# Kernel optimization log

Hardware: AMD Instinct MI355X
Metric: run time of the kernel (lower is better)

## Reference

```python
import jax, jax.numpy as jnp
import numpy as np

B, T, C = 4, 2048, 768
NH, NKV, HD = 12, 12, 64
RMS_EPS = 1e-6


def rms_norm(x):
    return x * jax.lax.rsqrt(jnp.mean(x * x, axis=-1, keepdims=True) + RMS_EPS)


def apply_rotary_emb(x, cos, sin):
    # x: [B,T,H,D], cos/sin: [T,D/2]
    d2 = x.shape[-1] // 2
    x1, x2 = x[..., :d2], x[..., d2:]
    c = cos[None, :, None, :]
    s = sin[None, :, None, :]
    return jnp.concatenate([x1 * c - x2 * s, x1 * s + x2 * c], axis=-1)


def setup_inputs() -> dict:
    key = jax.random.key(0)
    ks = jax.random.split(key, 10)
    inv_freq = 1.0 / (100000.0 ** (np.arange(0, HD, 2, dtype=np.float32) / HD))  # [HD/2]
    t = np.arange(T, dtype=np.float32)
    freqs = np.outer(t, inv_freq)  # [T, HD/2]
    return {
        "x": jax.random.normal(ks[0], (B, T, C), jnp.float32),
        "ve": jax.random.normal(ks[1], (B, T, C), jnp.float32),
        "cos": jnp.asarray(np.cos(freqs)),
        "sin": jnp.asarray(np.sin(freqs)),
        "Wq": jax.random.normal(ks[2], (C, C), jnp.float32) * (1.0 / np.sqrt(C)),
        "Wk": jax.random.normal(ks[3], (C, C), jnp.float32) * (1.0 / np.sqrt(C)),
        "Wv": jax.random.normal(ks[4], (C, C), jnp.float32) * (1.0 / np.sqrt(C)),
        "Wproj": jax.random.normal(ks[5], (C, C), jnp.float32) * (1.0 / np.sqrt(C)),
        "Wgate": jax.random.normal(ks[6], (NKV, 12), jnp.float32) * 0.1,
        "window_left": 1024,
    }


def reference(x, ve, cos, sin, Wq, Wk, Wv, Wproj, Wgate, window_left):
    q = (x @ Wq.T).reshape(B, T, NH, HD)
    k = (x @ Wk.T).reshape(B, T, NKV, HD)
    v = (x @ Wv.T).reshape(B, T, NKV, HD)

    # value-embedding gating (has_ve path): gate = 3*sigmoid(Linear(x[...,:12]))
    ve_h = ve.reshape(B, T, NKV, HD)
    gate = 3.0 * jax.nn.sigmoid(x[..., :12] @ Wgate.T)  # [B,T,NKV]
    v = v + gate[..., None] * ve_h

    q = apply_rotary_emb(q, cos, sin)
    k = apply_rotary_emb(k, cos, sin)
    q = rms_norm(q) * 1.2
    k = rms_norm(k) * 1.2

    # sliding-window causal bias
    row = jnp.arange(T)[:, None]
    col = jnp.arange(T)[None, :]
    mask = (row >= col) & ((row - col) <= window_left)
    bias = jnp.where(mask, 0.0, -1e9).astype(x.dtype)  # [T,T]

    scale = 1.0 / np.sqrt(HD)
    att = jnp.einsum("bqhd,bkhd->bhqk", q, k) * scale + bias[None, None]
    att = jax.nn.softmax(att, axis=-1)
    y = jnp.einsum("bhqk,bkhd->bqhd", att, v).reshape(B, T, C)
    return y @ Wproj.T
```

## Files before the change

kernel.cpp:

```cpp
#include <hip/hip_runtime.h>
#include <hip/hip_bf16.h>
#include <cstdint>
#include <cstddef>

#define B_  4
#define T_  2048
#define C_  768
#define NH_ 12
#define HD_ 64

typedef __bf16 bf16_t;
typedef __attribute__((ext_vector_type(8))) __bf16 bf16x8;
typedef __attribute__((ext_vector_type(4))) __bf16 bf16x4;
typedef __attribute__((ext_vector_type(4))) float floatx4;
typedef __attribute__((ext_vector_type(8))) unsigned short ushort8;
typedef __attribute__((ext_vector_type(4))) unsigned int uint4v;

#define MFMA16(a, b, c) __builtin_amdgcn_mfma_f32_16x16x32_bf16((a), (b), (c), 0, 0, 0)

#define SM_C1 0.18033688f
#define SM_C2 -17.3123405f

typedef const __attribute__((address_space(1))) uint8_t* gptr_t;
typedef __attribute__((address_space(3))) uint8_t* lptr_t;

static __device__ __forceinline__ void gld16(const void* g, void* l) {
    __builtin_amdgcn_global_load_lds((gptr_t)g, (lptr_t)l, 16, 0, 0);
}

__global__ __launch_bounds__(256) void cvt_all_kernel(
    const void* s0, const void* s1, const void* s2, const void* s3,
    const void* s4, const void* s5, const void* s6, const void* s7, const void* s8,
    bf16_t* d0, bf16_t* d1, bf16_t* d2, bf16_t* d3,
    bf16_t* d4, bf16_t* d5, bf16_t* d6, bf16_t* d7, bf16_t* d8)
{
    const void* srcs[9] = {s0, s1, s2, s3, s4, s5, s6, s7, s8};
    bf16_t*     dsts[9] = {d0, d1, d2, d3, d4, d5, d6, d7, d8};
    const int   ns[9]   = {B_*T_*C_, B_*T_*C_, T_*32, T_*32,
                           C_*C_, C_*C_, C_*C_, C_*C_, 144};
    const int t = blockIdx.y;
    const void* src = srcs[t];
    bf16_t*     dst = dsts[t];
    const int   nc  = ns[t] >> 3;
    const bool isf32 = (((const unsigned short*)s2)[0] == 0);
    const int stride = gridDim.x * 256;
    if (isf32) {
        const float* sf = (const float*)src;
        for (int i = blockIdx.x * 256 + threadIdx.x; i < nc; i += stride) {
            ushort8 o;
#pragma unroll
            for (int j = 0; j < 8; j++)
                o[j] = (unsigned short)__builtin_bit_cast(unsigned short,
                         (bf16_t)sf[i * 8 + j]);
            *(ushort8*)&dst[i * 8] = o;
        }
    } else {
        const uint4v* sb = (const uint4v*)src;
        uint4v* db = (uint4v*)dst;
        for (int i = blockIdx.x * 256 + threadIdx.x; i < nc; i += stride)
            db[i] = sb[i];
    }
}

template <bool OUT_BF16>
__device__ __forceinline__ void gemm_bt_tile(
    const bf16_t* __restrict__ A, const bf16_t* __restrict__ Bm,
    void* __restrict__ Cout, int m0, int n0, int K, int ldc)
{
    __shared__ bf16_t As[2][128 * 32];
    __shared__ bf16_t Bs[2][128 * 32];
    const int tid  = threadIdx.x;
    const int lane = tid & 63;
    const int wid  = tid >> 6;
    const int m16  = lane & 15;
    const int quad = lane >> 4;
    const int wm   = (wid >> 1) * 64;
    const int wn   = (wid & 1) * 64;
    const int srow = lane >> 2;
    const int soct = (lane & 3) * 8;

    floatx4 acc[4][4];
#pragma unroll
    for (int i = 0; i < 4; i++)
#pragma unroll
        for (int j = 0; j < 4; j++) acc[i][j] = (floatx4){0.f, 0.f, 0.f, 0.f};

    for (int k0 = 0; k0 < K; k0 += 64) {
        const bf16_t* ga0 = &A[(size_t)(m0 + 16 * wid + srow) * K + k0 + soct];
        const bf16_t* gb0 = &Bm[(size_t)(n0 + 16 * wid + srow) * K + k0 + soct];
        gld16(ga0,                       (bf16_t*)As[0] + wid * 512);
        gld16(ga0 + (size_t)64 * K,      (bf16_t*)As[0] + wid * 512 + 2048);
        gld16(gb0,                       (bf16_t*)Bs[0] + wid * 512);
        gld16(gb0 + (size_t)64 * K,      (bf16_t*)Bs[0] + wid * 512 + 2048);
        gld16(ga0 + 32,                  (bf16_t*)As[1] + wid * 512);
        gld16(ga0 + (size_t)64 * K + 32, (bf16_t*)As[1] + wid * 512 + 2048);
        gld16(gb0 + 32,                  (bf16_t*)Bs[1] + wid * 512);
        gld16(gb0 + (size_t)64 * K + 32, (bf16_t*)Bs[1] + wid * 512 + 2048);
        __syncthreads();
#pragma unroll
        for (int half = 0; half < 2; half++) {
            bf16x8 af[4], bfr[4];
#pragma unroll
            for (int i = 0; i < 4; i++)
                af[i] = *(const bf16x8*)&As[half][(wm + i * 16 + m16) * 32 + quad * 8];
#pragma unroll
            for (int j = 0; j < 4; j++)
                bfr[j] = *(const bf16x8*)&Bs[half][(wn + j * 16 + m16) * 32 + quad * 8];
#pragma unroll
            for (int i = 0; i < 4; i++)
#pragma unroll
                for (int j = 0; j < 4; j++)
                    acc[i][j] = MFMA16(af[i], bfr[j], acc[i][j]);
        }
        __syncthreads();
    }

#pragma unroll
    for (int i = 0; i < 4; i++) {
#pragma unroll
        for (int j = 0; j < 4; j++) {
            const int colg = n0 + wn + j * 16 + m16;
#pragma unroll
            for (int r = 0; r < 4; r++) {
                const int rowg = m0 + wm + i * 16 + quad * 4 + r;
                if (OUT_BF16)
                    ((bf16_t*)Cout)[(size_t)rowg * ldc + colg] = (bf16_t)acc[i][j][r];
                else
                    ((float*)Cout)[(size_t)rowg * ldc + colg] = acc[i][j][r];
            }
        }
    }
}

__global__ __launch_bounds__(256) void gemm_qkv_kernel(
    const bf16_t* __restrict__ xb,
    const bf16_t* __restrict__ wq, const bf16_t* __restrict__ wk,
    const bf16_t* __restrict__ wv,
    bf16_t* __restrict__ ql, bf16_t* __restrict__ kl, bf16_t* __restrict__ vl)
{
    const int sel = blockIdx.y / 6;
    const int nt  = blockIdx.y % 6;
    const bf16_t* Bm = (sel == 0) ? wq : (sel == 1) ? wk : wv;
    bf16_t* Cout     = (sel == 0) ? ql : (sel == 1) ? kl : vl;
    gemm_bt_tile<true>(xb, Bm, Cout, blockIdx.x * 128, nt * 128, C_, C_);
}

__global__ __launch_bounds__(256) void gemm_proj_kernel(
    const bf16_t* __restrict__ yb, const bf16_t* __restrict__ wp,
    void* __restrict__ out, const void* cos_raw)
{
    const bool isf32 = (((const unsigned short*)cos_raw)[0] == 0);
    if (isf32)
        gemm_bt_tile<false>(yb, wp, out, blockIdx.x * 128, blockIdx.y * 128, C_, C_);
    else
        gemm_bt_tile<true>(yb, wp, out, blockIdx.x * 128, blockIdx.y * 128, C_, C_);
}

__global__ __launch_bounds__(256) void qkv_post_kernel(
    const bf16_t* __restrict__ x, const bf16_t* __restrict__ ve,
    const bf16_t* __restrict__ cosp, const bf16_t* __restrict__ sinp,
    const bf16_t* __restrict__ wg,
    const bf16_t* __restrict__ ql, const bf16_t* __restrict__ kl,
    const bf16_t* __restrict__ vl,
    bf16_t* __restrict__ qb, bf16_t* __restrict__ kb, bf16_t* __restrict__ vt)
{
    const int t0 = blockIdx.x * 32;
    const int b  = blockIdx.y;
    const int w  = threadIdx.x >> 6;
    const int h  = blockIdx.z * 4 + w;
    const int d  = threadIdx.x & 63;
    __shared__ float vtile[4][32 * 65];
    float* vt_l = vtile[w];
    const float wgd = (d < 12) ? (float)wg[h * 12 + d] : 0.f;

    for (int c = 0; c < 32; c++) {
        const int t  = t0 + c;
        const int bt = b * T_ + t;
        const size_t lin = (size_t)bt * C_ + h * HD_ + d;
        float gx = (d < 12) ? (float)x[(size_t)bt * C_ + d] * wgd : 0.f;
        gx += __shfl_xor(gx, 1, 64); gx += __shfl_xor(gx, 2, 64);
        gx += __shfl_xor(gx, 4, 64); gx += __shfl_xor(gx, 8, 64);
        gx = __shfl(gx, 0, 64);
        const float gate = 3.f / (1.f + __expf(-gx));
        vt_l[c * 65 + d] = (float)vl[lin] + gate * (float)ve[lin];

        const float co = (float)cosp[t * 32 + (d & 31)];
        const float si = (float)sinp[t * 32 + (d & 31)];
        const size_t oidx = ((size_t)(b * NH_ + h) * T_ + t) * HD_ + d;
        {
            const float own = (float)ql[lin];
            const float oth = __shfl_xor(own, 32, 64);
            const float qr  = (d < 32) ? (own * co - oth * si) : (oth * si + own * co);
            float ss = qr * qr;
#pragma unroll
            for (int off = 1; off < 64; off <<= 1) ss += __shfl_xor(ss, off, 64);
            qb[oidx] = (bf16_t)(qr * rsqrtf(ss * (1.f / 64.f) + 1e-6f) * 1.2f);
        }
        {
            const float own = (float)kl[lin];
            const float oth = __shfl_xor(own, 32, 64);
            const float kr  = (d < 32) ? (own * co - oth * si) : (oth * si + own * co);
            float ss = kr * kr;
#pragma unroll
            for (int off = 1; off < 64; off <<= 1) ss += __shfl_xor(ss, off, 64);
            kb[oidx] = (bf16_t)(kr * rsqrtf(ss * (1.f / 64.f) + 1e-6f) * 1.2f);
        }
    }

    const int cc = threadIdx.x & 31;
    const int dh = (threadIdx.x >> 5) & 1;
    const int tp = t0 + ((((cc >> 2) & 3) << 3) | ((cc >> 4) << 2) | (cc & 3));
#pragma unroll 4
    for (int it = 0; it < 32; it++) {
        const int dd = it * 2 + dh;
        vt[((size_t)(b * NH_ + h) * HD_ + dd) * T_ + tp] =
            (bf16_t)vt_l[cc * 65 + dd];
    }
}

__global__ __launch_bounds__(256, 3) void attn_kernel(
    const bf16_t* __restrict__ Q, const bf16_t* __restrict__ Km,
    const bf16_t* __restrict__ Vtg, bf16_t* __restrict__ Y,
    const int* __restrict__ wl)
{
    const int bx   = blockIdx.x;
    const int bh   = blockIdx.y;
    const int gsel = bh >> 4;
    int qblk;
    if (gsel == 0)      qblk = bx;
    else if (gsel == 1) qblk = 15 - bx;
    else                qblk = (int)((0xECA8642013579BDFull >> (bx * 4)) & 0xF);
    const int q0 = qblk * 128;
    const int b  = bh / NH_;
    const int h  = bh % NH_;
    const int window = wl[0];
    const int tid  = threadIdx.x;
    const int wid  = tid >> 6;
    const int lane = tid & 63;
    const int m16  = lane & 15;
    const int quad = lane >> 4;
    const int qw   = q0 + wid * 32;

    const size_t base = (size_t)bh * T_ * HD_;
    const bf16_t* Qb  = Q + base;
    const bf16_t* Kb  = Km + base;
    const bf16_t* Vb  = Vtg + base;

    __shared__ bf16_t Ks[2][64 * 64];
    __shared__ bf16_t Vs[2][64 * 64];

    bf16x8 qf[2][2];
#pragma unroll
    for (int mt = 0; mt < 2; mt++)
#pragma unroll
        for (int ks = 0; ks < 2; ks++)
            qf[mt][ks] = *(const bf16x8*)
                &Qb[(size_t)(qw + mt * 16 + m16) * HD_ + ks * 32 + quad * 8];

    const int srow = tid >> 2;
    const int soct = tid & 3;
    const int g0   = 2 * soct, g1 = 2 * soct + 1;
    const int kd0  = srow * 64 + ((g0 ^ (srow & 7)) << 3);
    const int kd1  = srow * 64 + ((g1 ^ (srow & 7)) << 3);
    int rsw[2];
#pragma unroll
    for (int ks = 0; ks < 2; ks++)
        rsw[ks] = (((ks * 4 + quad) ^ (m16 & 7)) << 3);

    int lo = q0 - window;
    if (lo < 0) lo = 0;
    lo &= ~63;
    const int nch = (q0 + 128 - lo) >> 6;

    floatx4 accO[2][4];
#pragma unroll
    for (int mt = 0; mt < 2; mt++)
#pragma unroll
        for (int dt = 0; dt < 4; dt++) accO[mt][dt] = (floatx4){0.f, 0.f, 0.f, 0.f};
    float lsum[2] = {0.f, 0.f};
    const bf16x4 zero4 = {(bf16_t)0.f, (bf16_t)0.f, (bf16_t)0.f, (bf16_t)0.f};

    bf16x8 ka0 = *(const bf16x8*)&Kb[(size_t)(lo + srow) * HD_ + g0 * 8];
    bf16x8 ka1 = *(const bf16x8*)&Kb[(size_t)(lo + srow) * HD_ + g1 * 8];
    bf16x8 va0 = *(const bf16x8*)&Vb[(size_t)srow * T_ + lo + g0 * 8];
    bf16x8 va1 = *(const bf16x8*)&Vb[(size_t)srow * T_ + lo + g1 * 8];
    *(bf16x8*)&Ks[0][kd0] = ka0;
    *(bf16x8*)&Ks[0][kd1] = ka1;
    *(bf16x8*)&Vs[0][kd0] = va0;
    *(bf16x8*)&Vs[0][kd1] = va1;

    for (int ic = 0; ic < nch; ic++) {
        const int kc = lo + ic * 64;
        const bool more = (ic + 1 < nch);
        if (more) {
            const int kn = kc + 64;
            ka0 = *(const bf16x8*)&Kb[(size_t)(kn + srow) * HD_ + g0 * 8];
            ka1 = *(const bf16x8*)&Kb[(size_t)(kn + srow) * HD_ + g1 * 8];
            va0 = *(const bf16x8*)&Vb[(size_t)srow * T_ + kn + g0 * 8];
            va1 = *(const bf16x8*)&Vb[(size_t)srow * T_ + kn + g1 * 8];
        }
        __syncthreads();
        const int buf = ic & 1;

        const bool skip = (kc > qw + 31) || (kc + 63 < qw - window);
        if (!skip) {
            bf16x8 kf[4][2];
#pragma unroll
            for (int nt = 0; nt < 4; nt++) {
                const int rb = (nt * 16 + m16) * 64;
                kf[nt][0] = *(const bf16x8*)&Ks[buf][rb + rsw[0]];
                kf[nt][1] = *(const bf16x8*)&Ks[buf][rb + rsw[1]];
            }
            bf16x4 pk[2][4];
            unsigned livemask = 0;
#pragma unroll
            for (int mt = 0; mt < 2; mt++) {
                const int qmin = qw + mt * 16, qmax = qmin + 15;
                float lacc = 0.f;
#pragma unroll
                for (int nt = 0; nt < 4; nt++) {
                    const int kmin = kc + nt * 16, kmax = kmin + 15;
                    if (kmin > qmax || kmax < qmin - window) {
                        pk[mt][nt] = zero4;
                        continue;
                    }
                    livemask |= 1u << (mt * 4 + nt);
                    floatx4 z = (floatx4){0.f, 0.f, 0.f, 0.f};
                    z = MFMA16(kf[nt][0], qf[mt][0], z);
                    z = MFMA16(kf[nt][1], qf[mt][1], z);
                    const bool edge = (kmax > qmin) || (kmin < qmax - window);
                    const int query = qmin + m16;
                    bf16x4 t4;
#pragma unroll
                    for (int r = 0; r < 4; r++) {
                        float p = __builtin_amdgcn_exp2f(
                            fmaf(z[r], SM_C1, SM_C2));
                        if (edge) {
                            const int key = kmin + quad * 4 + r;
                            const bool ok = (key <= query) &&
                                            (query - key <= window);
                            p = ok ? p : 0.f;
                        }
                        t4[r] = (bf16_t)p;
                        lacc += p;
                    }
                    pk[mt][nt] = t4;
                }
                lsum[mt] += lacc;
            }
#pragma unroll
            for (int pr = 0; pr < 2; pr++) {
                const unsigned pm0 = (livemask >> (2 * pr)) & 3u;
                const unsigned pm1 = (livemask >> (4 + 2 * pr)) & 3u;
                if (!(pm0 | pm1)) continue;
                const bf16x8 pa0 = __builtin_shufflevector(
                    pk[0][2 * pr], pk[0][2 * pr + 1], 0, 1, 2, 3, 4, 5, 6, 7);
                const bf16x8 pa1 = __builtin_shufflevector(
                    pk[1][2 * pr], pk[1][2 * pr + 1], 0, 1, 2, 3, 4, 5, 6, 7);
                const int vco = (((pr * 4 + quad) ^ (m16 & 7)) << 3);
#pragma unroll
                for (int dt = 0; dt < 4; dt++) {
                    const bf16x8 vf = *(const bf16x8*)
                        &Vs[buf][(dt * 16 + m16) * 64 + vco];
                    if (pm0) accO[0][dt] = MFMA16(pa0, vf, accO[0][dt]);
                    if (pm1) accO[1][dt] = MFMA16(pa1, vf, accO[1][dt]);
                }
            }
        }

        if (more) {
            const int nb = buf ^ 1;
            *(bf16x8*)&Ks[nb][kd0] = ka0;
            *(bf16x8*)&Ks[nb][kd1] = ka1;
            *(bf16x8*)&Vs[nb][kd0] = va0;
            *(bf16x8*)&Vs[nb][kd1] = va1;
        }
    }

#pragma unroll
    for (int mt = 0; mt < 2; mt++) {
        float red = lsum[mt];
        red += __shfl_xor(red, 16, 64);
        red += __shfl_xor(red, 32, 64);
#pragma unroll
        for (int r = 0; r < 4; r++) {
            const float lq  = __shfl(red, quad * 4 + r, 64);
            const float inv = 1.f / lq;
            const int   tq  = qw + mt * 16 + quad * 4 + r;
#pragma unroll
            for (int dt = 0; dt < 4; dt++)
                Y[((size_t)b * T_ + tq) * C_ + h * HD_ + dt * 16 + m16] =
                    (bf16_t)(accO[mt][dt][r] * inv);
        }
    }
}

extern "C" void kernel_launch(void* const* d_in, const int* in_sizes, int n_in,
                              void* d_out, int out_size, void* d_ws, size_t ws_size,
                              hipStream_t stream)
{
    const void* x_raw   = d_in[0];
    const void* ve_raw  = d_in[1];
    const void* cos_raw = d_in[2];
    const void* sin_raw = d_in[3];
    const void* wq_raw  = d_in[4];
    const void* wk_raw  = d_in[5];
    const void* wv_raw  = d_in[6];
    const void* wp_raw  = d_in[7];
    const void* wg_raw  = d_in[8];
    const int*  wl      = (const int*)d_in[9];

    const size_t NTC = (size_t)B_ * T_ * C_;
    const size_t WSZ = (size_t)C_ * C_;

    bf16_t* ws  = (bf16_t*)d_ws;
    bf16_t* xb  = ws;
    bf16_t* veb = xb + NTC;
    bf16_t* cb  = veb + NTC;
    bf16_t* sb  = cb + T_ * 32;
    bf16_t* wqb = sb + T_ * 32;
    bf16_t* wkb = wqb + WSZ;
    bf16_t* wvb = wkb + WSZ;
    bf16_t* wpb = wvb + WSZ;
    bf16_t* wgb = wpb + WSZ;
    bf16_t* ql  = wgb + 256;
    bf16_t* kl  = ql + NTC;
    bf16_t* vl  = kl + NTC;
    bf16_t* qb  = vl + NTC;
    bf16_t* kb  = qb + NTC;
    bf16_t* vt  = kb + NTC;
    bf16_t* yb  = ql;

    cvt_all_kernel<<<dim3(1024, 9), 256, 0, stream>>>(
        x_raw, ve_raw, cos_raw, sin_raw, wq_raw, wk_raw, wv_raw, wp_raw, wg_raw,
        xb, veb, cb, sb, wqb, wkb, wvb, wpb, wgb);

    gemm_qkv_kernel<<<dim3(64, 18), 256, 0, stream>>>(xb, wqb, wkb, wvb, ql, kl, vl);

    qkv_post_kernel<<<dim3(T_ / 32, B_, 3), 256, 0, stream>>>(
        xb, veb, cb, sb, wgb, ql, kl, vl, qb, kb, vt);

    attn_kernel<<<dim3(16, 48), 256, 0, stream>>>(qb, kb, vt, yb, wl);

    gemm_proj_kernel<<<dim3(64, 6), 256, 0, stream>>>(yb, wpb, d_out, cos_raw);
}
```

Baseline: 257.3 us.

## Fuse RoPE, RMSNorm and value gating into QKV GEMM epilogue

Removes the separate qkv_post kernel. The QKV GEMM epilogue now applies rotary embedding and RMSNorm to Q/K inside registers, using a shuffle reduction across the 64-wide head. For V it adds the sigmoid-gated value embedding and writes the transposed layout. Attention now reads Q/K in the [B,T,C] layout, and the conversion kernel is skipped when inputs are already bf16. This removes a full round trip of the Q, K and V intermediates through global memory, at the cost of a heavier GEMM epilogue and strided attention loads.

```diff
diff --git a/kernel.cpp b/kernel.cpp
--- a/kernel.cpp
+++ b/kernel.cpp
@@ -14,7 +14,6 @@
 typedef __attribute__((ext_vector_type(4))) __bf16 bf16x4;
 typedef __attribute__((ext_vector_type(4))) float floatx4;
 typedef __attribute__((ext_vector_type(8))) unsigned short ushort8;
-typedef __attribute__((ext_vector_type(4))) unsigned int uint4v;
 
 #define MFMA16(a, b, c) __builtin_amdgcn_mfma_f32_16x16x32_bf16((a), (b), (c), 0, 0, 0)
 
@@ -26,6 +25,13 @@
 
 static __device__ __forceinline__ void gld16(const void* g, void* l) {
     __builtin_amdgcn_global_load_lds((gptr_t)g, (lptr_t)l, 16, 0, 0);
+}
+
+static __device__ __forceinline__ float bfl(unsigned p) {
+    return __builtin_bit_cast(float, p << 16);
+}
+static __device__ __forceinline__ float bfh(unsigned p) {
+    return __builtin_bit_cast(float, p & 0xffff0000u);
 }
 
 __global__ __launch_bounds__(256) void cvt_all_kernel(
@@ -34,31 +40,191 @@
     bf16_t* d0, bf16_t* d1, bf16_t* d2, bf16_t* d3,
     bf16_t* d4, bf16_t* d5, bf16_t* d6, bf16_t* d7, bf16_t* d8)
 {
+    const bool isf32 = (((const unsigned short*)s2)[0] == 0);
+    if (!isf32) return;
     const void* srcs[9] = {s0, s1, s2, s3, s4, s5, s6, s7, s8};
     bf16_t*     dsts[9] = {d0, d1, d2, d3, d4, d5, d6, d7, d8};
     const int   ns[9]   = {B_*T_*C_, B_*T_*C_, T_*32, T_*32,
                            C_*C_, C_*C_, C_*C_, C_*C_, 144};
     const int t = blockIdx.y;
-    const void* src = srcs[t];
+    const float* sf = (const float*)srcs[t];
     bf16_t*     dst = dsts[t];
     const int   nc  = ns[t] >> 3;
-    const bool isf32 = (((const unsigned short*)s2)[0] == 0);
     const int stride = gridDim.x * 256;
-    if (isf32) {
-        const float* sf = (const float*)src;
-        for (int i = blockIdx.x * 256 + threadIdx.x; i < nc; i += stride) {
-            ushort8 o;
-#pragma unroll
-            for (int j = 0; j < 8; j++)
-                o[j] = (unsigned short)__builtin_bit_cast(unsigned short,
-                         (bf16_t)sf[i * 8 + j]);
-            *(ushort8*)&dst[i * 8] = o;
+    for (int i = blockIdx.x * 256 + threadIdx.x; i < nc; i += stride) {
+        ushort8 o;
+#pragma unroll
+        for (int j = 0; j < 8; j++)
+            o[j] = (unsigned short)__builtin_bit_cast(unsigned short,
+                     (bf16_t)sf[i * 8 + j]);
+        *(ushort8*)&dst[i * 8] = o;
+    }
+}
+
+__global__ __launch_bounds__(256) void gemm_qkv_fused(
+    const void* xr,  const bf16_t* xc,
+    const void* wqr, const bf16_t* wqc,
+    const void* wkr, const bf16_t* wkc,
+    const void* wvr, const bf16_t* wvc,
+    const void* cr,  const bf16_t* ccv,
+    const void* sr,  const bf16_t* scv,
+    const void* ver, const bf16_t* vec,
+    const void* wgr, const bf16_t* wgc,
+    bf16_t* qn, bf16_t* kn, bf16_t* vt)
+{
+    __shared__ alignas(16) char sm[36864];
+    const bool f32 = (((const unsigned short*)cr)[0] == 0);
+    const bf16_t* X  = f32 ? xc  : (const bf16_t*)xr;
+    const bf16_t* WQ = f32 ? wqc : (const bf16_t*)wqr;
+    const bf16_t* WK = f32 ? wkc : (const bf16_t*)wkr;
+    const bf16_t* WV = f32 ? wvc : (const bf16_t*)wvr;
+    const bf16_t* CC = f32 ? ccv : (const bf16_t*)cr;
+    const bf16_t* SS = f32 ? scv : (const bf16_t*)sr;
+    const bf16_t* VE = f32 ? vec : (const bf16_t*)ver;
+    const bf16_t* WG = f32 ? wgc : (const bf16_t*)wgr;
+
+    const int sel = blockIdx.y / 6;
+    const int nt  = blockIdx.y % 6;
+    const int m0  = blockIdx.x * 128;
+    const int n0  = nt * 128;
+    const bf16_t* Bm = (sel == 0) ? WQ : (sel == 1) ? WK : WV;
+
+    bf16_t* As = (bf16_t*)sm;
+    bf16_t* Bs = (bf16_t*)(sm + 16384);
+
+    const int tid  = threadIdx.x;
+    const int lane = tid & 63;
+    const int wid  = tid >> 6;
+    const int m16  = lane & 15;
+    const int quad = lane >> 4;
+    const int wm   = (wid >> 1) * 64;
+    const int wn   = (wid & 1) * 64;
+    const int srow = lane >> 2;
+    const int soct = (lane & 3) * 8;
+
+    floatx4 acc[4][4];
+#pragma unroll
+    for (int i = 0; i < 4; i++)
+#pragma unroll
+        for (int j = 0; j < 4; j++) acc[i][j] = (floatx4){0.f, 0.f, 0.f, 0.f};
+
+    for (int k0 = 0; k0 < C_; k0 += 64) {
+        const bf16_t* ga0 = &X[(size_t)(m0 + 16 * wid + srow) * C_ + k0 + soct];
+        const bf16_t* gb0 = &Bm[(size_t)(n0 + 16 * wid + srow) * C_ + k0 + soct];
+        gld16(ga0,                        As + wid * 512);
+        gld16(ga0 + (size_t)64 * C_,      As + wid * 512 + 2048);
+        gld16(gb0,                        Bs + wid * 512);
+        gld16(gb0 + (size_t)64 * C_,      Bs + wid * 512 + 2048);
+        gld16(ga0 + 32,                   As + 4096 + wid * 512);
+        gld16(ga0 + (size_t)64 * C_ + 32, As + 4096 + wid * 512 + 2048);
+        gld16(gb0 + 32,                   Bs + 4096 + wid * 512);
+        gld16(gb0 + (size_t)64 * C_ + 32, Bs + 4096 + wid * 512 + 2048);
+        __syncthreads();
+#pragma unroll
+        for (int half = 0; half < 2; half++) {
+            bf16x8 af[4], bfr[4];
+#pragma unroll
+            for (int i = 0; i < 4; i++)
+                af[i] = *(const bf16x8*)&As[half * 4096 + (wm + i * 16 + m16) * 32 + quad * 8];
+#pragma unroll
+            for (int j = 0; j < 4; j++)
+                bfr[j] = *(const bf16x8*)&Bs[half * 4096 + (wn + j * 16 + m16) * 32 + quad * 8];
+#pragma unroll
+            for (int i = 0; i < 4; i++)
+#pragma unroll
+                for (int j = 0; j < 4; j++)
+                    acc[i][j] = MFMA16(af[i], bfr[j], acc[i][j]);
+        }
+        __syncthreads();
+    }
+
+    if (sel < 2) {
+        unsigned* csT = (unsigned*)sm;
+        const int tbase = m0 & 2047;
+        for (int idx = tid; idx < 128 * 32; idx += 256) {
+            const int rr = idx >> 5, dd = idx & 31;
+            const unsigned cv = ((const unsigned short*)CC)[(tbase + rr) * 32 + dd];
+            const unsigned sv = ((const unsigned short*)SS)[(tbase + rr) * 32 + dd];
+            csT[rr * 33 + dd] = cv | (sv << 16);
+        }
+        __syncthreads();
+        bf16_t* OUT = (sel == 0) ? qn : kn;
+#pragma unroll
+        for (int i = 0; i < 4; i++) {
+            float c0[4], s0[4], c1[4], s1[4];
+#pragma unroll
+            for (int r = 0; r < 4; r++) {
+                const int rl = wm + i * 16 + quad * 4 + r;
+                const unsigned p0 = csT[rl * 33 + m16];
+                const unsigned p1 = csT[rl * 33 + 16 + m16];
+                c0[r] = bfl(p0); s0[r] = bfh(p0);
+                c1[r] = bfl(p1); s1[r] = bfh(p1);
+            }
+            floatx4 r0, r1, r2, r3;
+            float ss[4];
+#pragma unroll
+            for (int r = 0; r < 4; r++) {
+                r0[r] = acc[i][0][r] * c0[r] - acc[i][2][r] * s0[r];
+                r1[r] = acc[i][1][r] * c1[r] - acc[i][3][r] * s1[r];
+                r2[r] = acc[i][0][r] * s0[r] + acc[i][2][r] * c0[r];
+                r3[r] = acc[i][1][r] * s1[r] + acc[i][3][r] * c1[r];
+                ss[r] = r0[r]*r0[r] + r1[r]*r1[r] + r2[r]*r2[r] + r3[r]*r3[r];
+            }
+#pragma unroll
+            for (int r = 0; r < 4; r++) {
+#pragma unroll
+                for (int off = 1; off < 16; off <<= 1)
+                    ss[r] += __shfl_xor(ss[r], off, 64);
+            }
+#pragma unroll
+            for (int r = 0; r < 4; r++) {
+                const float scl = rsqrtf(ss[r] * (1.f / 64.f) + 1e-6f) * 1.2f;
+                const size_t rowoff = (size_t)(m0 + wm + i * 16 + quad * 4 + r) * C_
+                                      + n0 + wn + m16;
+                OUT[rowoff]      = (bf16_t)(r0[r] * scl);
+                OUT[rowoff + 16] = (bf16_t)(r1[r] * scl);
+                OUT[rowoff + 32] = (bf16_t)(r2[r] * scl);
+                OUT[rowoff + 48] = (bf16_t)(r3[r] * scl);
+            }
         }
     } else {
-        const uint4v* sb = (const uint4v*)src;
-        uint4v* db = (uint4v*)dst;
-        for (int i = blockIdx.x * 256 + threadIdx.x; i < nc; i += stride)
-            db[i] = sb[i];
+        bf16_t* veT = (bf16_t*)sm;
+        float*  gT  = (float*)(sm + 34816);
+        for (int idx = tid; idx < 2048; idx += 256) {
+            const int rr = idx >> 4, ch = idx & 15;
+            *(bf16x8*)&veT[rr * 136 + ch * 8] =
+                *(const bf16x8*)&VE[(size_t)(m0 + rr) * C_ + n0 + ch * 8];
+        }
+        {
+            const int row = tid & 127, hh = tid >> 7;
+            const int head = nt * 2 + hh;
+            float g = 0.f;
+#pragma unroll
+            for (int j2 = 0; j2 < 12; j2++)
+                g += (float)X[(size_t)(m0 + row) * C_ + j2] * (float)WG[head * 12 + j2];
+            gT[hh * 128 + row] = 3.f / (1.f + __expf(-g));
+        }
+        __syncthreads();
+        const int hh2  = wn >> 6;
+        const int head = nt * 2 + hh2;
+        const int bb = m0 >> 11, t0 = m0 & 2047;
+#pragma unroll
+        for (int i = 0; i < 4; i++) {
+            const floatx4 gr = *(const floatx4*)&gT[hh2 * 128 + wm + i * 16 + quad * 4];
+            const int tslot = t0 + wm + (i >> 1) * 32 + quad * 8 + (i & 1) * 4;
+#pragma unroll
+            for (int j = 0; j < 4; j++) {
+                bf16x4 o;
+#pragma unroll
+                for (int r = 0; r < 4; r++) {
+                    const float vef = (float)veT[(wm + i * 16 + quad * 4 + r) * 136
+                                                 + wn + j * 16 + m16];
+                    o[r] = (bf16_t)(acc[i][j][r] + gr[r] * vef);
+                }
+                *(bf16x4*)&vt[((size_t)(bb * NH_ + head) * HD_ + j * 16 + m16) * T_
+                              + tslot] = o;
+            }
+        }
     }
 }
 
@@ -114,7 +280,6 @@
         }
         __syncthreads();
     }
-
 #pragma unroll
     for (int i = 0; i < 4; i++) {
 #pragma unroll
@@ -132,90 +297,16 @@
     }
 }
 
-__global__ __launch_bounds__(256) void gemm_qkv_kernel(
-    const bf16_t* __restrict__ xb,
-    const bf16_t* __restrict__ wq, const bf16_t* __restrict__ wk,
-    const bf16_t* __restrict__ wv,
-    bf16_t* __restrict__ ql, bf16_t* __restrict__ kl, bf16_t* __restrict__ vl)
+__global__ __launch_bounds__(256) void gemm_proj_kernel(
+    const bf16_t* __restrict__ yb, const void* wpr, const bf16_t* wpc,
+    void* __restrict__ out, const void* cr)
 {
-    const int sel = blockIdx.y / 6;
-    const int nt  = blockIdx.y % 6;
-    const bf16_t* Bm = (sel == 0) ? wq : (sel == 1) ? wk : wv;
-    bf16_t* Cout     = (sel == 0) ? ql : (sel == 1) ? kl : vl;
-    gemm_bt_tile<true>(xb, Bm, Cout, blockIdx.x * 128, nt * 128, C_, C_);
-}
-
-__global__ __launch_bounds__(256) void gemm_proj_kernel(
-    const bf16_t* __restrict__ yb, const bf16_t* __restrict__ wp,
-    void* __restrict__ out, const void* cos_raw)
-{
-    const bool isf32 = (((const unsigned short*)cos_raw)[0] == 0);
-    if (isf32)
-        gemm_bt_tile<false>(yb, wp, out, blockIdx.x * 128, blockIdx.y * 128, C_, C_);
+    const bool f32 = (((const unsigned short*)cr)[0] == 0);
+    const bf16_t* WP = f32 ? wpc : (const bf16_t*)wpr;
+    if (f32)
+        gemm_bt_tile<false>(yb, WP, out, blockIdx.x * 128, blockIdx.y * 128, C_, C_);
     else
-        gemm_bt_tile<true>(yb, wp, out, blockIdx.x * 128, blockIdx.y * 128, C_, C_);
-}
-
-__global__ __launch_bounds__(256) void qkv_post_kernel(
-    const bf16_t* __restrict__ x, const bf16_t* __restrict__ ve,
-    const bf16_t* __restrict__ cosp, const bf16_t* __restrict__ sinp,
-    const bf16_t* __restrict__ wg,
-    const bf16_t* __restrict__ ql, const bf16_t* __restrict__ kl,
-    const bf16_t* __restrict__ vl,
-    bf16_t* __restrict__ qb, bf16_t* __restrict__ kb, bf16_t* __restrict__ vt)
-{
-    const int t0 = blockIdx.x * 32;
-    const int b  = blockIdx.y;
-    const int w  = threadIdx.x >> 6;
-    const int h  = blockIdx.z * 4 + w;
-    const int d  = threadIdx.x & 63;
-    __shared__ float vtile[4][32 * 65];
-    float* vt_l = vtile[w];
-    const float wgd = (d < 12) ? (float)wg[h * 12 + d] : 0.f;
-
-    for (int c = 0; c < 32; c++) {
-        const int t  = t0 + c;
-        const int bt = b * T_ + t;
-        const size_t lin = (size_t)bt * C_ + h * HD_ + d;
-        float gx = (d < 12) ? (float)x[(size_t)bt * C_ + d] * wgd : 0.f;
-        gx += __shfl_xor(gx, 1, 64); gx += __shfl_xor(gx, 2, 64);
-        gx += __shfl_xor(gx, 4, 64); gx += __shfl_xor(gx, 8, 64);
-        gx = __shfl(gx, 0, 64);
-        const float gate = 3.f / (1.f + __expf(-gx));
-        vt_l[c * 65 + d] = (float)vl[lin] + gate * (float)ve[lin];
-
-        const float co = (float)cosp[t * 32 + (d & 31)];
-        const float si = (float)sinp[t * 32 + (d & 31)];
-        const size_t oidx = ((size_t)(b * NH_ + h) * T_ + t) * HD_ + d;
-        {
-            const float own = (float)ql[lin];
-            const float oth = __shfl_xor(own, 32, 64);
-            const float qr  = (d < 32) ? (own * co - oth * si) : (oth * si + own * co);
-            float ss = qr * qr;
-#pragma unroll
-            for (int off = 1; off < 64; off <<= 1) ss += __shfl_xor(ss, off, 64);
-            qb[oidx] = (bf16_t)(qr * rsqrtf(ss * (1.f / 64.f) + 1e-6f) * 1.2f);
-        }
-        {
-            const float own = (float)kl[lin];
-            const float oth = __shfl_xor(own, 32, 64);
-            const float kr  = (d < 32) ? (own * co - oth * si) : (oth * si + own * co);
-            float ss = kr * kr;
-#pragma unroll
-            for (int off = 1; off < 64; off <<= 1) ss += __shfl_xor(ss, off, 64);
-            kb[oidx] = (bf16_t)(kr * rsqrtf(ss * (1.f / 64.f) + 1e-6f) * 1.2f);
-        }
-    }
-
-    const int cc = threadIdx.x & 31;
-    const int dh = (threadIdx.x >> 5) & 1;
-    const int tp = t0 + ((((cc >> 2) & 3) << 3) | ((cc >> 4) << 2) | (cc & 3));
-#pragma unroll 4
-    for (int it = 0; it < 32; it++) {
-        const int dd = it * 2 + dh;
-        vt[((size_t)(b * NH_ + h) * HD_ + dd) * T_ + tp] =
-            (bf16_t)vt_l[cc * 65 + dd];
-    }
+        gemm_bt_tile<true>(yb, WP, out, blockIdx.x * 128, blockIdx.y * 128, C_, C_);
 }
 
 __global__ __launch_bounds__(256, 3) void attn_kernel(
@@ -241,10 +332,9 @@
     const int quad = lane >> 4;
     const int qw   = q0 + wid * 32;
 
-    const size_t base = (size_t)bh * T_ * HD_;
-    const bf16_t* Qb  = Q + base;
-    const bf16_t* Kb  = Km + base;
-    const bf16_t* Vb  = Vtg + base;
+    const bf16_t* Qb = Q + (size_t)b * T_ * C_ + h * HD_;
+    const bf16_t* Kb = Km + (size_t)b * T_ * C_ + h * HD_;
+    const bf16_t* Vb = Vtg + (size_t)bh * HD_ * T_;
 
     __shared__ bf16_t Ks[2][64 * 64];
     __shared__ bf16_t Vs[2][64 * 64];
@@ -255,7 +345,7 @@
 #pragma unroll
         for (int ks = 0; ks < 2; ks++)
             qf[mt][ks] = *(const bf16x8*)
-                &Qb[(size_t)(qw + mt * 16 + m16) * HD_ + ks * 32 + quad * 8];
+                &Qb[(size_t)(qw + mt * 16 + m16) * C_ + ks * 32 + quad * 8];
 
     const int srow = tid >> 2;
     const int soct = tid & 3;
@@ -280,8 +370,8 @@
     float lsum[2] = {0.f, 0.f};
     const bf16x4 zero4 = {(bf16_t)0.f, (bf16_t)0.f, (bf16_t)0.f, (bf16_t)0.f};
 
-    bf16x8 ka0 = *(const bf16x8*)&Kb[(size_t)(lo + srow) * HD_ + g0 * 8];
-    bf16x8 ka1 = *(const bf16x8*)&Kb[(size_t)(lo + srow) * HD_ + g1 * 8];
+    bf16x8 ka0 = *(const bf16x8*)&Kb[(size_t)(lo + srow) * C_ + g0 * 8];
+    bf16x8 ka1 = *(const bf16x8*)&Kb[(size_t)(lo + srow) * C_ + g1 * 8];
     bf16x8 va0 = *(const bf16x8*)&Vb[(size_t)srow * T_ + lo + g0 * 8];
     bf16x8 va1 = *(const bf16x8*)&Vb[(size_t)srow * T_ + lo + g1 * 8];
     *(bf16x8*)&Ks[0][kd0] = ka0;
@@ -293,11 +383,11 @@
         const int kc = lo + ic * 64;
         const bool more = (ic + 1 < nch);
         if (more) {
-            const int kn = kc + 64;
-            ka0 = *(const bf16x8*)&Kb[(size_t)(kn + srow) * HD_ + g0 * 8];
-            ka1 = *(const bf16x8*)&Kb[(size_t)(kn + srow) * HD_ + g1 * 8];
-            va0 = *(const bf16x8*)&Vb[(size_t)srow * T_ + kn + g0 * 8];
-            va1 = *(const bf16x8*)&Vb[(size_t)srow * T_ + kn + g1 * 8];
+            const int kn2 = kc + 64;
+            ka0 = *(const bf16x8*)&Kb[(size_t)(kn2 + srow) * C_ + g0 * 8];
+            ka1 = *(const bf16x8*)&Kb[(size_t)(kn2 + srow) * C_ + g1 * 8];
+            va0 = *(const bf16x8*)&Vb[(size_t)srow * T_ + kn2 + g0 * 8];
+            va1 = *(const bf16x8*)&Vb[(size_t)srow * T_ + kn2 + g1 * 8];
         }
         __syncthreads();
         const int buf = ic & 1;
@@ -423,24 +513,21 @@
     bf16_t* wvb = wkb + WSZ;
     bf16_t* wpb = wvb + WSZ;
     bf16_t* wgb = wpb + WSZ;
-    bf16_t* ql  = wgb + 256;
-    bf16_t* kl  = ql + NTC;
-    bf16_t* vl  = kl + NTC;
-    bf16_t* qb  = vl + NTC;
-    bf16_t* kb  = qb + NTC;
-    bf16_t* vt  = kb + NTC;
-    bf16_t* yb  = ql;
-
-    cvt_all_kernel<<<dim3(1024, 9), 256, 0, stream>>>(
+    bf16_t* qn  = wgb + 256;
+    bf16_t* kn  = qn + NTC;
+    bf16_t* vt  = kn + NTC;
+    bf16_t* yb  = vt + NTC;
+
+    cvt_all_kernel<<<dim3(128, 9), 256, 0, stream>>>(
         x_raw, ve_raw, cos_raw, sin_raw, wq_raw, wk_raw, wv_raw, wp_raw, wg_raw,
         xb, veb, cb, sb, wqb, wkb, wvb, wpb, wgb);
 
-    gemm_qkv_kernel<<<dim3(64, 18), 256, 0, stream>>>(xb, wqb, wkb, wvb, ql, kl, vl);
-
-    qkv_post_kernel<<<dim3(T_ / 32, B_, 3), 256, 0, stream>>>(
-        xb, veb, cb, sb, wgb, ql, kl, vl, qb, kb, vt);
-
-    attn_kernel<<<dim3(16, 48), 256, 0, stream>>>(qb, kb, vt, yb, wl);
-
-    gemm_proj_kernel<<<dim3(64, 6), 256, 0, stream>>>(yb, wpb, d_out, cos_raw);
-}
+    gemm_qkv_fused<<<dim3(64, 18), 256, 0, stream>>>(
+        x_raw, xb, wq_raw, wqb, wk_raw, wkb, wv_raw, wvb,
+        cos_raw, cb, sin_raw, sb, ve_raw, veb, wg_raw, wgb,
+        qn, kn, vt);
+
+    attn_kernel<<<dim3(16, 48), 256, 0, stream>>>(qn, kn, vt, yb, wl);
+
+    gemm_proj_kernel<<<dim3(64, 6), 256, 0, stream>>>(yb, wp_raw, wpb, d_out, cos_raw);
+}
```

Result: faster. 247.9 us (-3.6%).
